# Optimization experiments

Measured on AMD Instinct MI355X. Metric: run time of the kernel, lower is better.

## Reference

```python
import jax, jax.numpy as jnp
import numpy as np

NEG_INF = 1e9  # matches module's -1000000000.0 masking constant


def setup_inputs() -> dict:
    key = jax.random.key(0)
    kq, kv = jax.random.split(key)
    B, T, D = 4, 2048, 1024
    query = jax.random.normal(kq, (B, T, D), dtype=jnp.float32)
    value = jax.random.normal(kv, (B, T, D), dtype=jnp.float32)
    return {"query": query, "value": value}


def reference(query, value):
    # key defaults to value (len(inputs) == 2 path)
    k = value
    # dot-product scores (canonical Keras Attention _calculate_scores)
    scores = jnp.einsum("bqd,bkd->bqk", query, k)  # [B, Tq, Tv]
    Tq, Tv = scores.shape[-2], scores.shape[-1]
    # causal lower-triangular mask over last two dims (row >= col)
    causal_mask = jnp.tril(jnp.ones((Tq, Tv), dtype=bool))  # [Tq, Tv]
    # scores -= 1e9 * (~mask), then softmax (eval mode: no dropout)
    scores = scores - NEG_INF * (~causal_mask).astype(scores.dtype)
    weights = jax.nn.softmax(scores, axis=-1)
    result = jnp.einsum("bqv,bvd->bqd", weights, value)
    return result
```

## Files before the change

### kernel.cpp

```cpp
#include <hip/hip_runtime.h>
#include <hip/hip_fp16.h>

typedef _Float16 half8 __attribute__((ext_vector_type(8)));
typedef float    floatx4 __attribute__((ext_vector_type(4)));
typedef unsigned int uintx4 __attribute__((ext_vector_type(4)));

#define MFMA16(a, b, c) __builtin_amdgcn_mfma_f32_16x16x32_f16((a), (b), (c), 0, 0, 0)

constexpr int T_ = 2048;
constexpr int D_ = 1024;
constexpr int NB = 4;
constexpr int NTILE = 136;
constexpr size_t PT_ELEMS = 16384;

__device__ __forceinline__ half8 cvt8(floatx4 a, floatx4 b) {
  half8 h;
  h[0] = (_Float16)a[0]; h[1] = (_Float16)a[1]; h[2] = (_Float16)a[2]; h[3] = (_Float16)a[3];
  h[4] = (_Float16)b[0]; h[5] = (_Float16)b[1]; h[6] = (_Float16)b[2]; h[7] = (_Float16)b[3];
  return h;
}

__device__ __forceinline__ void gl16(const void* g, void* l) {
  __builtin_amdgcn_global_load_lds(
      (const __attribute__((address_space(1))) void*)g,
      (__attribute__((address_space(3))) void*)l, 16, 0, 0);
}

__global__ __launch_bounds__(256) void cast_h(const float* __restrict__ X,
                                              _Float16* __restrict__ Xh) {
  const size_t i = ((size_t)blockIdx.x * 256 + threadIdx.x) * 8;
  *(half8*)(Xh + i) = cvt8(*(const floatx4*)(X + i), *(const floatx4*)(X + i + 4));
}

__global__ __launch_bounds__(256) void build_vt(const float* __restrict__ V,
                                                _Float16* __restrict__ VhT) {
  __shared__ _Float16 tile[64][65];
  const int bid = blockIdx.x;
  const int b = bid & 3, tt = (bid >> 2) & 31, dd = bid >> 7;
  const float* Vb = V + ((size_t)b * T_ + tt * 64) * D_ + dd * 64;
#pragma unroll
  for (int k = 0; k < 16; ++k) {
    const int e = k * 256 + threadIdx.x, r = e >> 6, c = e & 63;
    tile[r][c] = (_Float16)Vb[(size_t)r * D_ + c];
  }
  __syncthreads();
#pragma unroll
  for (int k = 0; k < 16; ++k) {
    const int e = k * 256 + threadIdx.x, dr = e >> 6, tc = e & 63;
    VhT[((size_t)b * D_ + dd * 64 + dr) * T_ + tt * 64 + tc] = tile[tc][dr];
  }
}

__global__ __launch_bounds__(256, 2) void sgemm(const _Float16* __restrict__ Qh,
                                                const _Float16* __restrict__ Vh,
                                                _Float16* __restrict__ Pt,
                                                float* __restrict__ mg,
                                                float* __restrict__ lg) {
  extern __shared__ __align__(16) char lds[];
  char* As = lds;
  char* Bs = lds + 32768;
  const int tid = threadIdx.x;
  const int w = tid >> 6, l = tid & 63, l15 = l & 15, hi = l >> 4;
  const int wr = (w >> 1) * 64, wc = (w & 1) * 64;

  const int b = (int)(blockIdx.x & 3);
  int rem = (int)(blockIdx.x >> 2), j = 0;
  while (rem >= 16 - j) { rem -= 16 - j; ++j; }
  const int i = j + rem;

  const _Float16* Qb = Qh + ((size_t)(b * T_ + i * 128)) * D_;
  const _Float16* Vb = Vh + ((size_t)(b * T_ + j * 128)) * D_;
  const int srow = w * 32 + (l >> 4);
  char* Adst = As + w * 8192;
  char* Bdst = Bs + w * 8192;

  floatx4 acc[4][4];
#pragma unroll
  for (int mi = 0; mi < 4; ++mi)
#pragma unroll
    for (int ni = 0; ni < 4; ++ni) acc[mi][ni] = (floatx4){0.f, 0.f, 0.f, 0.f};

  for (int s = 0; s < 8; ++s) {
#pragma unroll
    for (int q = 0; q < 8; ++q) {
      const int r0 = srow + q * 4;
      const int sc = ((l & 15) ^ (r0 & 15)) * 8;
      gl16(Qb + (size_t)r0 * D_ + s * 128 + sc, Adst + q * 1024);
      gl16(Vb + (size_t)r0 * D_ + s * 128 + sc, Bdst + q * 1024);
    }
    __syncthreads();
#pragma unroll
    for (int s32 = 0; s32 < 4; ++s32) {
      half8 af[4], bb[4];
#pragma unroll
      for (int mi = 0; mi < 4; ++mi) {
        const int row = wr + mi * 16 + l15;
        af[mi] = *(const half8*)(As + row * 256 + (((s32 * 4 + hi) ^ (row & 15)) << 4));
      }
#pragma unroll
      for (int ni = 0; ni < 4; ++ni) {
        const int row = wc + ni * 16 + l15;
        bb[ni] = *(const half8*)(Bs + row * 256 + (((s32 * 4 + hi) ^ (row & 15)) << 4));
      }
#pragma unroll
      for (int mi = 0; mi < 4; ++mi)
#pragma unroll
        for (int ni = 0; ni < 4; ++ni)
          acc[mi][ni] = MFMA16(af[mi], bb[ni], acc[mi][ni]);
    }
    __syncthreads();
  }

  float* Mex = (float*)Bs;
  float* Lex = (float*)(Bs + 1024);

  if (i == j) {
#pragma unroll
    for (int mi = 0; mi < 4; ++mi)
#pragma unroll
      for (int ni = 0; ni < 4; ++ni) {
        const int col = wc + ni * 16 + l15;
        const int row0 = wr + mi * 16 + 4 * hi;
#pragma unroll
        for (int r = 0; r < 4; ++r)
          if (col > row0 + r) acc[mi][ni][r] = -1e30f;
      }
  }

  floatx4 mrow[4];
#pragma unroll
  for (int mi = 0; mi < 4; ++mi) {
#pragma unroll
    for (int r = 0; r < 4; ++r)
      mrow[mi][r] = fmaxf(fmaxf(acc[mi][0][r], acc[mi][1][r]),
                          fmaxf(acc[mi][2][r], acc[mi][3][r]));
#pragma unroll
    for (int off = 1; off < 16; off <<= 1)
#pragma unroll
      for (int r = 0; r < 4; ++r)
        mrow[mi][r] = fmaxf(mrow[mi][r], __shfl_xor(mrow[mi][r], off));
  }
  if (l15 == 0) {
#pragma unroll
    for (int mi = 0; mi < 4; ++mi)
      *(floatx4*)&Mex[(w & 1) * 128 + wr + mi * 16 + 4 * hi] = mrow[mi];
  }
  __syncthreads();
#pragma unroll
  for (int mi = 0; mi < 4; ++mi) {
    const floatx4 m0 = *(const floatx4*)&Mex[wr + mi * 16 + 4 * hi];
    const floatx4 m1 = *(const floatx4*)&Mex[128 + wr + mi * 16 + 4 * hi];
#pragma unroll
    for (int r = 0; r < 4; ++r) mrow[mi][r] = fmaxf(m0[r], m1[r]);
  }

  floatx4 lsum[4];
#pragma unroll
  for (int mi = 0; mi < 4; ++mi) {
    lsum[mi] = (floatx4){0.f, 0.f, 0.f, 0.f};
    const int row0 = wr + mi * 16 + 4 * hi;
#pragma unroll
    for (int ni = 0; ni < 4; ++ni) {
      const int col = wc + ni * 16 + l15;
#pragma unroll
      for (int r = 0; r < 4; ++r) {
        const float p = __expf(acc[mi][ni][r] - mrow[mi][r]);
        lsum[mi][r] += p;
        *(_Float16*)(As + (row0 + r) * 256 + col * 2) = (_Float16)p;
      }
    }
#pragma unroll
    for (int off = 1; off < 16; off <<= 1)
#pragma unroll
      for (int r = 0; r < 4; ++r) lsum[mi][r] += __shfl_xor(lsum[mi][r], off);
  }
  if (l15 == 0) {
#pragma unroll
    for (int mi = 0; mi < 4; ++mi)
      *(floatx4*)&Lex[(w & 1) * 128 + wr + mi * 16 + 4 * hi] = lsum[mi];
  }
  __syncthreads();

  if (((w & 1) == 0) && l15 == 0) {
    const size_t base = ((size_t)(b * 16 + j)) * 2048 + i * 128;
#pragma unroll
    for (int mi = 0; mi < 4; ++mi) {
      const int r0 = wr + mi * 16 + 4 * hi;
      const floatx4 l0 = *(const floatx4*)&Lex[r0];
      const floatx4 l1 = *(const floatx4*)&Lex[128 + r0];
#pragma unroll
      for (int r = 0; r < 4; ++r) {
        mg[base + r0 + r] = mrow[mi][r];
        lg[base + r0 + r] = l0[r] + l1[r];
      }
    }
  }
  _Float16* Pg = Pt + (size_t)(b * NTILE + ((i * (i + 1)) >> 1) + j) * PT_ELEMS;
  const int drow = tid >> 1, dhalf = tid & 1;
#pragma unroll
  for (int k = 0; k < 8; ++k) {
    const int c = k ^ (tid & 7);
    const uintx4 v = *(const uintx4*)(As + drow * 256 + dhalf * 128 + c * 16);
    *(uintx4*)((char*)Pg + drow * 256 + dhalf * 128 + c * 16) = v;
  }
}

__global__ __launch_bounds__(256) void combine(const float* __restrict__ mg,
                                               const float* __restrict__ lg,
                                               _Float16* __restrict__ ah,
                                               float* __restrict__ linv) {
  const int gid = (int)(blockIdx.x * 256 + threadIdx.x);
  const int b = gid >> 11, row = gid & 2047, i = row >> 7;
  const size_t mb = (size_t)b * 32768 + row;
  float M = -1e30f;
  for (int j = 0; j <= i; ++j) M = fmaxf(M, mg[mb + (size_t)j * 2048]);
  float L = 0.f;
  for (int j = 0; j <= i; ++j) {
    const float a = __expf(mg[mb + (size_t)j * 2048] - M);
    L += a * lg[mb + (size_t)j * 2048];
    ah[((size_t)b * 2048 + row) * 16 + j] = (_Float16)a;
  }
  linv[b * 2048 + row] = 1.0f / L;
}

__global__ __launch_bounds__(256, 2) void pv(const _Float16* __restrict__ Pt,
                                             const _Float16* __restrict__ VhT,
                                             const _Float16* __restrict__ ah,
                                             const float* __restrict__ linv,
                                             float* __restrict__ O) {
  extern __shared__ __align__(16) char lds[];
  char* As = lds;
  char* Bs = lds + 32768;
  const int tid = threadIdx.x;
  const int w = tid >> 6, l = tid & 63, l15 = l & 15, hi = l >> 4;
  const int wr = (w >> 1) * 64, wc = (w & 1) * 64;

  const int b = (int)(blockIdx.x & 3), t = (int)(blockIdx.x >> 2);
  const int r_ = t >> 3;
  const int i = (r_ < 8) ? (15 - r_) : (r_ - 8);
  const int nc = t & 7;
  const int ns = i + 1;

  const _Float16* Pb = Pt + (size_t)(b * NTILE + ((i * (i + 1)) >> 1)) * PT_ELEMS;
  const _Float16* Vt = VhT + ((size_t)(b * D_ + nc * 128)) * T_;
  const int srow = w * 32 + (l >> 4);
  char* Adst = As + w * 8192;
  char* Bdst = Bs + w * 8192;

  floatx4 acc[4][4];
#pragma unroll
  for (int mi = 0; mi < 4; ++mi)
#pragma unroll
    for (int ni = 0; ni < 4; ++ni) acc[mi][ni] = (floatx4){0.f, 0.f, 0.f, 0.f};

  for (int s = 0; s < ns; ++s) {
    _Float16 aw[4];
#pragma unroll
    for (int mi = 0; mi < 4; ++mi)
      aw[mi] = ah[((size_t)(b * 2048 + i * 128 + wr + mi * 16 + l15)) * 16 + s];
#pragma unroll
    for (int q = 0; q < 8; ++q) {
      const int r0 = srow + q * 4;
      const int sc = ((l & 15) ^ (r0 & 15)) * 8;
      gl16(Pb + (size_t)s * PT_ELEMS + (size_t)r0 * 128 + sc, Adst + q * 1024);
      gl16(Vt + (size_t)r0 * T_ + s * 128 + sc, Bdst + q * 1024);
    }
    __syncthreads();
#pragma unroll
    for (int s32 = 0; s32 < 4; ++s32) {
      half8 af[4], bb[4];
#pragma unroll
      for (int mi = 0; mi < 4; ++mi) {
        const int row = wr + mi * 16 + l15;
        af[mi] = *(const half8*)(As + row * 256 + (((s32 * 4 + hi) ^ (row & 15)) << 4));
        af[mi] *= aw[mi];
      }
#pragma unroll
      for (int ni = 0; ni < 4; ++ni) {
        const int row = wc + ni * 16 + l15;
        bb[ni] = *(const half8*)(Bs + row * 256 + (((s32 * 4 + hi) ^ (row & 15)) << 4));
      }
#pragma unroll
      for (int mi = 0; mi < 4; ++mi)
#pragma unroll
        for (int ni = 0; ni < 4; ++ni)
          acc[mi][ni] = MFMA16(af[mi], bb[ni], acc[mi][ni]);
    }
    __syncthreads();
  }

  float* Ob = O + ((size_t)b * T_ + i * 128) * D_ + nc * 128;
#pragma unroll
  for (int mi = 0; mi < 4; ++mi)
#pragma unroll
    for (int r = 0; r < 4; ++r) {
      const int rl = wr + mi * 16 + 4 * hi + r;
      const float iv = linv[b * 2048 + i * 128 + rl];
#pragma unroll
      for (int ni = 0; ni < 4; ++ni)
        Ob[(size_t)rl * D_ + wc + ni * 16 + l15] = acc[mi][ni][r] * iv;
    }
}

__global__ __launch_bounds__(256) void attn_fb(const float* __restrict__ Q,
                                               const float* __restrict__ V,
                                               float* __restrict__ O) {
  __shared__ float sc[2048];
  __shared__ float red[4];
  const int b = (int)(blockIdx.x >> 11), m = (int)(blockIdx.x & 2047);
  const int tid = threadIdx.x;
  const float* Qr = Q + ((size_t)b * T_ + m) * D_;
  for (int kv = tid; kv <= m; kv += 256) {
    const float* Vr = V + ((size_t)b * T_ + kv) * D_;
    float s = 0.f;
    for (int d = 0; d < D_; d += 4) {
      floatx4 q4 = *(const floatx4*)(Qr + d), v4 = *(const floatx4*)(Vr + d);
      s += q4[0] * v4[0] + q4[1] * v4[1] + q4[2] * v4[2] + q4[3] * v4[3];
    }
    sc[kv] = s;
  }
  __syncthreads();
  float mx = -1e30f;
  for (int kv = tid; kv <= m; kv += 256) mx = fmaxf(mx, sc[kv]);
#pragma unroll
  for (int off = 1; off < 64; off <<= 1) mx = fmaxf(mx, __shfl_xor(mx, off));
  if ((tid & 63) == 0) red[tid >> 6] = mx;
  __syncthreads();
  mx = fmaxf(fmaxf(red[0], red[1]), fmaxf(red[2], red[3]));
  __syncthreads();
  float sum = 0.f;
  for (int kv = tid; kv <= m; kv += 256) { float p = __expf(sc[kv] - mx); sc[kv] = p; sum += p; }
#pragma unroll
  for (int off = 1; off < 64; off <<= 1) sum += __shfl_xor(sum, off);
  __syncthreads();
  if ((tid & 63) == 0) red[tid >> 6] = sum;
  __syncthreads();
  const float inv = 1.0f / (red[0] + red[1] + red[2] + red[3]);
  float* Or = O + ((size_t)b * T_ + m) * D_;
  const int d = tid * 4;
  floatx4 o = {0.f, 0.f, 0.f, 0.f};
  for (int kv = 0; kv <= m; ++kv) {
    const float p = sc[kv];
    const floatx4 v4 = *(const floatx4*)(V + ((size_t)b * T_ + kv) * D_ + d);
    o[0] += p * v4[0]; o[1] += p * v4[1]; o[2] += p * v4[2]; o[3] += p * v4[3];
  }
  o[0] *= inv; o[1] *= inv; o[2] *= inv; o[3] *= inv;
  *(floatx4*)(Or + d) = o;
}

extern "C" void kernel_launch(void* const* d_in, const int* in_sizes, int n_in,
                              void* d_out, int out_size, void* d_ws, size_t ws_size,
                              hipStream_t stream) {
  const float* q = (const float*)d_in[0];
  const float* v = (const float*)d_in[1];
  float* out = (float*)d_out;

  const size_t OFF_VH = 16777216;
  const size_t OFF_P  = 33554432;
  const size_t OFF_M  = OFF_P + (size_t)NB * NTILE * PT_ELEMS * 2;
  const size_t OFF_LT = OFF_M + 524288;
  const size_t OFF_AH = OFF_LT + 524288;
  const size_t OFF_LI = OFF_AH + 262144;
  const size_t NEED   = OFF_LI + 32768;

  if (ws_size >= NEED) {
    _Float16* qh = (_Float16*)d_ws;
    _Float16* vh = (_Float16*)((char*)d_ws + OFF_VH);
    _Float16* pt = (_Float16*)((char*)d_ws + OFF_P);
    float* mg = (float*)((char*)d_ws + OFF_M);
    float* lg = (float*)((char*)d_ws + OFF_LT);
    _Float16* ah = (_Float16*)((char*)d_ws + OFF_AH);
    float* li = (float*)((char*)d_ws + OFF_LI);
    hipFuncSetAttribute((const void*)sgemm, hipFuncAttributeMaxDynamicSharedMemorySize, 65536);
    hipFuncSetAttribute((const void*)pv, hipFuncAttributeMaxDynamicSharedMemorySize, 65536);
    cast_h<<<dim3(4096), dim3(256), 0, stream>>>(q, qh);
    cast_h<<<dim3(4096), dim3(256), 0, stream>>>(v, vh);
    sgemm<<<dim3(NB * NTILE), dim3(256), 65536, stream>>>(qh, vh, pt, mg, lg);
    combine<<<dim3(32), dim3(256), 0, stream>>>(mg, lg, ah, li);
    build_vt<<<dim3(2048), dim3(256), 0, stream>>>(v, qh);
    pv<<<dim3(512), dim3(256), 65536, stream>>>(pt, qh, ah, li, out);
  } else {
    attn_fb<<<dim3(NB * T_), dim3(256), 0, stream>>>(q, v, out);
  }
}
```

Before: 118.2 us.

## Shrink PV tiles to 128x64 with smaller k-steps and fuse cast kernels

The two fp16 cast launches are merged into one prep kernel that handles Q and V, with each thread converting 16 elements. The PV kernel moves from 128x128 output tiles with 128-wide k-steps to 128x64 tiles with 64-wide k-steps and static 24KB LDS. That doubles the grid to 1024 blocks, raises the occupancy hint to 4 blocks per SM, and interleaves tile rows to balance causal work. The goal is better occupancy and load balance on the triangular PV work, at the cost of more k-iterations, more barriers and less operand reuse per block.

```diff
diff --git a/kernel.cpp b/kernel.cpp
--- a/kernel.cpp
+++ b/kernel.cpp
@@ -26,10 +26,16 @@
       (__attribute__((address_space(3))) void*)l, 16, 0, 0);
 }
 
-__global__ __launch_bounds__(256) void cast_h(const float* __restrict__ X,
-                                              _Float16* __restrict__ Xh) {
-  const size_t i = ((size_t)blockIdx.x * 256 + threadIdx.x) * 8;
-  *(half8*)(Xh + i) = cvt8(*(const floatx4*)(X + i), *(const floatx4*)(X + i + 4));
+__global__ __launch_bounds__(256) void prep(const float* __restrict__ Q,
+                                            const float* __restrict__ V,
+                                            _Float16* __restrict__ Qh,
+                                            _Float16* __restrict__ Vh) {
+  const int bid = blockIdx.x;
+  const float* src = (bid < 2048) ? Q : V;
+  _Float16* dst = (bid < 2048) ? Qh : Vh;
+  const size_t i = ((size_t)(bid & 2047) * 256 + threadIdx.x) * 16;
+  *(half8*)(dst + i)     = cvt8(*(const floatx4*)(src + i),     *(const floatx4*)(src + i + 4));
+  *(half8*)(dst + i + 8) = cvt8(*(const floatx4*)(src + i + 8), *(const floatx4*)(src + i + 12));
 }
 
 __global__ __launch_bounds__(256) void build_vt(const float* __restrict__ V,
@@ -223,65 +229,69 @@
   linv[b * 2048 + row] = 1.0f / L;
 }
 
-__global__ __launch_bounds__(256, 2) void pv(const _Float16* __restrict__ Pt,
+__global__ __launch_bounds__(256, 4) void pv(const _Float16* __restrict__ Pt,
                                              const _Float16* __restrict__ VhT,
                                              const _Float16* __restrict__ ah,
                                              const float* __restrict__ linv,
                                              float* __restrict__ O) {
-  extern __shared__ __align__(16) char lds[];
-  char* As = lds;
-  char* Bs = lds + 32768;
+  __shared__ __align__(16) char As[16384];
+  __shared__ __align__(16) char Bs[8192];
   const int tid = threadIdx.x;
   const int w = tid >> 6, l = tid & 63, l15 = l & 15, hi = l >> 4;
-  const int wr = (w >> 1) * 64, wc = (w & 1) * 64;
-
-  const int b = (int)(blockIdx.x & 3), t = (int)(blockIdx.x >> 2);
-  const int r_ = t >> 3;
-  const int i = (r_ < 8) ? (15 - r_) : (r_ - 8);
-  const int nc = t & 7;
-  const int ns = i + 1;
-
-  const _Float16* Pb = Pt + (size_t)(b * NTILE + ((i * (i + 1)) >> 1)) * PT_ELEMS;
-  const _Float16* Vt = VhT + ((size_t)(b * D_ + nc * 128)) * T_;
-  const int srow = w * 32 + (l >> 4);
-  char* Adst = As + w * 8192;
-  char* Bdst = Bs + w * 8192;
-
-  floatx4 acc[4][4];
-#pragma unroll
-  for (int mi = 0; mi < 4; ++mi)
+  const int wr = w * 32;
+
+  const int b = (int)(blockIdx.x & 3);
+  const int u = (int)(blockIdx.x >> 2);
+  const int iidx = (u + (u >> 4)) & 15;
+  const int i = (iidx < 8) ? (15 - iidx) : (iidx - 8);
+  const int nc = u >> 4;
+  const int ns = (i + 1) * 2;
+
+  const _Float16* Pp = Pt + (size_t)(b * NTILE + ((i * (i + 1)) >> 1)) * PT_ELEMS;
+  const _Float16* Vt = VhT + ((size_t)(b * D_ + nc * 64)) * T_;
+
+  floatx4 acc[2][4];
+#pragma unroll
+  for (int mi = 0; mi < 2; ++mi)
 #pragma unroll
     for (int ni = 0; ni < 4; ++ni) acc[mi][ni] = (floatx4){0.f, 0.f, 0.f, 0.f};
 
   for (int s = 0; s < ns; ++s) {
-    _Float16 aw[4];
-#pragma unroll
-    for (int mi = 0; mi < 4; ++mi)
-      aw[mi] = ah[((size_t)(b * 2048 + i * 128 + wr + mi * 16 + l15)) * 16 + s];
-#pragma unroll
-    for (int q = 0; q < 8; ++q) {
-      const int r0 = srow + q * 4;
-      const int sc = ((l & 15) ^ (r0 & 15)) * 8;
-      gl16(Pb + (size_t)s * PT_ELEMS + (size_t)r0 * 128 + sc, Adst + q * 1024);
-      gl16(Vt + (size_t)r0 * T_ + s * 128 + sc, Bdst + q * 1024);
+    const int jt = s >> 1, half = s & 1;
+    _Float16 aw[2];
+#pragma unroll
+    for (int mi = 0; mi < 2; ++mi)
+      aw[mi] = ah[((size_t)(b * 2048 + i * 128 + wr + mi * 16 + l15)) * 16 + jt];
+#pragma unroll
+    for (int q = 0; q < 4; ++q) {
+      const int ar = w * 32 + q * 8 + (l >> 3);
+      gl16(Pp + (size_t)jt * PT_ELEMS + (size_t)ar * 128 + half * 64 +
+               ((l & 7) ^ (ar & 7)) * 8,
+           As + w * 4096 + q * 1024);
+    }
+#pragma unroll
+    for (int q = 0; q < 2; ++q) {
+      const int br = w * 16 + q * 8 + (l >> 3);
+      gl16(Vt + (size_t)br * T_ + s * 64 + ((l & 7) ^ (br & 7)) * 8,
+           Bs + w * 2048 + q * 1024);
     }
     __syncthreads();
 #pragma unroll
-    for (int s32 = 0; s32 < 4; ++s32) {
-      half8 af[4], bb[4];
-#pragma unroll
-      for (int mi = 0; mi < 4; ++mi) {
+    for (int s32 = 0; s32 < 2; ++s32) {
+      half8 af[2], bb[4];
+#pragma unroll
+      for (int mi = 0; mi < 2; ++mi) {
         const int row = wr + mi * 16 + l15;
-        af[mi] = *(const half8*)(As + row * 256 + (((s32 * 4 + hi) ^ (row & 15)) << 4));
+        af[mi] = *(const half8*)(As + row * 128 + (((s32 * 4 + hi) ^ (row & 7)) << 4));
         af[mi] *= aw[mi];
       }
 #pragma unroll
       for (int ni = 0; ni < 4; ++ni) {
-        const int row = wc + ni * 16 + l15;
-        bb[ni] = *(const half8*)(Bs + row * 256 + (((s32 * 4 + hi) ^ (row & 15)) << 4));
-      }
-#pragma unroll
-      for (int mi = 0; mi < 4; ++mi)
+        const int row = ni * 16 + l15;
+        bb[ni] = *(const half8*)(Bs + row * 128 + (((s32 * 4 + hi) ^ (row & 7)) << 4));
+      }
+#pragma unroll
+      for (int mi = 0; mi < 2; ++mi)
 #pragma unroll
         for (int ni = 0; ni < 4; ++ni)
           acc[mi][ni] = MFMA16(af[mi], bb[ni], acc[mi][ni]);
@@ -289,16 +299,16 @@
     __syncthreads();
   }
 
-  float* Ob = O + ((size_t)b * T_ + i * 128) * D_ + nc * 128;
-#pragma unroll
-  for (int mi = 0; mi < 4; ++mi)
+  float* Ob = O + ((size_t)b * T_ + i * 128) * D_ + nc * 64;
+#pragma unroll
+  for (int mi = 0; mi < 2; ++mi)
 #pragma unroll
     for (int r = 0; r < 4; ++r) {
       const int rl = wr + mi * 16 + 4 * hi + r;
       const float iv = linv[b * 2048 + i * 128 + rl];
 #pragma unroll
       for (int ni = 0; ni < 4; ++ni)
-        Ob[(size_t)rl * D_ + wc + ni * 16 + l15] = acc[mi][ni][r] * iv;
+        Ob[(size_t)rl * D_ + ni * 16 + l15] = acc[mi][ni][r] * iv;
     }
 }
 
@@ -372,13 +382,11 @@
     _Float16* ah = (_Float16*)((char*)d_ws + OFF_AH);
     float* li = (float*)((char*)d_ws + OFF_LI);
     hipFuncSetAttribute((const void*)sgemm, hipFuncAttributeMaxDynamicSharedMemorySize, 65536);
-    hipFuncSetAttribute((const void*)pv, hipFuncAttributeMaxDynamicSharedMemorySize, 65536);
-    cast_h<<<dim3(4096), dim3(256), 0, stream>>>(q, qh);
-    cast_h<<<dim3(4096), dim3(256), 0, stream>>>(v, vh);
+    prep<<<dim3(4096), dim3(256), 0, stream>>>(q, v, qh, vh);
     sgemm<<<dim3(NB * NTILE), dim3(256), 65536, stream>>>(qh, vh, pt, mg, lg);
     combine<<<dim3(32), dim3(256), 0, stream>>>(mg, lg, ah, li);
     build_vt<<<dim3(2048), dim3(256), 0, stream>>>(v, qh);
-    pv<<<dim3(512), dim3(256), 65536, stream>>>(pt, qh, ah, li, out);
+    pv<<<dim3(1024), dim3(256), 0, stream>>>(pt, qh, ah, li, out);
   } else {
     attn_fb<<<dim3(NB * T_), dim3(256), 0, stream>>>(q, v, out);
   }
```

Result: slower. 120.7 us (+2.1%).

## Fuse Q/V casts into one kernel and halve PV k-step LDS footprint

Applied to the files above, without the earlier changes.

The two fp16 cast launches become one prep kernel in which each thread converts 16 elements. The pv kernel now steps through K in 64-wide chunks instead of 128, so it uses 32 KB of static LDS instead of 64 KB dynamic, and launch bounds allow 3 blocks per CU for more occupancy. The swizzle is adjusted to match 128-byte rows. The trade-off is twice as many loop iterations and barriers per tile, and less data reuse per barrier.

```diff
diff --git a/kernel.cpp b/kernel.cpp
--- a/kernel.cpp
+++ b/kernel.cpp
@@ -26,10 +26,16 @@
       (__attribute__((address_space(3))) void*)l, 16, 0, 0);
 }
 
-__global__ __launch_bounds__(256) void cast_h(const float* __restrict__ X,
-                                              _Float16* __restrict__ Xh) {
-  const size_t i = ((size_t)blockIdx.x * 256 + threadIdx.x) * 8;
-  *(half8*)(Xh + i) = cvt8(*(const floatx4*)(X + i), *(const floatx4*)(X + i + 4));
+__global__ __launch_bounds__(256) void prep(const float* __restrict__ Q,
+                                            const float* __restrict__ V,
+                                            _Float16* __restrict__ Qh,
+                                            _Float16* __restrict__ Vh) {
+  const int bid = blockIdx.x;
+  const float* src = (bid < 2048) ? Q : V;
+  _Float16* dst = (bid < 2048) ? Qh : Vh;
+  const size_t i = ((size_t)(bid & 2047) * 256 + threadIdx.x) * 16;
+  *(half8*)(dst + i)     = cvt8(*(const floatx4*)(src + i),     *(const floatx4*)(src + i + 4));
+  *(half8*)(dst + i + 8) = cvt8(*(const floatx4*)(src + i + 8), *(const floatx4*)(src + i + 12));
 }
 
 __global__ __launch_bounds__(256) void build_vt(const float* __restrict__ V,
@@ -223,29 +229,26 @@
   linv[b * 2048 + row] = 1.0f / L;
 }
 
-__global__ __launch_bounds__(256, 2) void pv(const _Float16* __restrict__ Pt,
+__global__ __launch_bounds__(256, 3) void pv(const _Float16* __restrict__ Pt,
                                              const _Float16* __restrict__ VhT,
                                              const _Float16* __restrict__ ah,
                                              const float* __restrict__ linv,
                                              float* __restrict__ O) {
-  extern __shared__ __align__(16) char lds[];
-  char* As = lds;
-  char* Bs = lds + 32768;
+  __shared__ __align__(16) char As[16384];
+  __shared__ __align__(16) char Bs[16384];
   const int tid = threadIdx.x;
   const int w = tid >> 6, l = tid & 63, l15 = l & 15, hi = l >> 4;
   const int wr = (w >> 1) * 64, wc = (w & 1) * 64;
 
   const int b = (int)(blockIdx.x & 3), t = (int)(blockIdx.x >> 2);
   const int r_ = t >> 3;
-  const int i = (r_ < 8) ? (15 - r_) : (r_ - 8);
+  const int I = (r_ < 8) ? (15 - r_) : (r_ - 8);
   const int nc = t & 7;
-  const int ns = i + 1;
-
-  const _Float16* Pb = Pt + (size_t)(b * NTILE + ((i * (i + 1)) >> 1)) * PT_ELEMS;
+  const int ns = (I + 1) * 2;
+
+  const _Float16* Pp = Pt + (size_t)(b * NTILE + ((I * (I + 1)) >> 1)) * PT_ELEMS;
   const _Float16* Vt = VhT + ((size_t)(b * D_ + nc * 128)) * T_;
-  const int srow = w * 32 + (l >> 4);
-  char* Adst = As + w * 8192;
-  char* Bdst = Bs + w * 8192;
+  const int srow = w * 32 + (l >> 3);
 
   floatx4 acc[4][4];
 #pragma unroll
@@ -254,31 +257,33 @@
     for (int ni = 0; ni < 4; ++ni) acc[mi][ni] = (floatx4){0.f, 0.f, 0.f, 0.f};
 
   for (int s = 0; s < ns; ++s) {
+    const int jt = s >> 1, half = s & 1;
     _Float16 aw[4];
 #pragma unroll
     for (int mi = 0; mi < 4; ++mi)
-      aw[mi] = ah[((size_t)(b * 2048 + i * 128 + wr + mi * 16 + l15)) * 16 + s];
-#pragma unroll
-    for (int q = 0; q < 8; ++q) {
-      const int r0 = srow + q * 4;
-      const int sc = ((l & 15) ^ (r0 & 15)) * 8;
-      gl16(Pb + (size_t)s * PT_ELEMS + (size_t)r0 * 128 + sc, Adst + q * 1024);
-      gl16(Vt + (size_t)r0 * T_ + s * 128 + sc, Bdst + q * 1024);
+      aw[mi] = ah[((size_t)(b * 2048 + I * 128 + wr + mi * 16 + l15)) * 16 + jt];
+#pragma unroll
+    for (int q = 0; q < 4; ++q) {
+      const int ar = srow + q * 8;
+      const int sc = ((l & 7) ^ (ar & 7)) * 8;
+      gl16(Pp + (size_t)jt * PT_ELEMS + (size_t)ar * 128 + half * 64 + sc,
+           As + w * 4096 + q * 1024);
+      gl16(Vt + (size_t)ar * T_ + s * 64 + sc, Bs + w * 4096 + q * 1024);
     }
     __syncthreads();
 #pragma unroll
-    for (int s32 = 0; s32 < 4; ++s32) {
+    for (int s32 = 0; s32 < 2; ++s32) {
       half8 af[4], bb[4];
 #pragma unroll
       for (int mi = 0; mi < 4; ++mi) {
         const int row = wr + mi * 16 + l15;
-        af[mi] = *(const half8*)(As + row * 256 + (((s32 * 4 + hi) ^ (row & 15)) << 4));
+        af[mi] = *(const half8*)(As + row * 128 + (((s32 * 4 + hi) ^ (row & 7)) << 4));
         af[mi] *= aw[mi];
       }
 #pragma unroll
       for (int ni = 0; ni < 4; ++ni) {
         const int row = wc + ni * 16 + l15;
-        bb[ni] = *(const half8*)(Bs + row * 256 + (((s32 * 4 + hi) ^ (row & 15)) << 4));
+        bb[ni] = *(const half8*)(Bs + row * 128 + (((s32 * 4 + hi) ^ (row & 7)) << 4));
       }
 #pragma unroll
       for (int mi = 0; mi < 4; ++mi)
@@ -289,13 +294,13 @@
     __syncthreads();
   }
 
-  float* Ob = O + ((size_t)b * T_ + i * 128) * D_ + nc * 128;
+  float* Ob = O + ((size_t)b * T_ + I * 128) * D_ + nc * 128;
 #pragma unroll
   for (int mi = 0; mi < 4; ++mi)
 #pragma unroll
     for (int r = 0; r < 4; ++r) {
       const int rl = wr + mi * 16 + 4 * hi + r;
-      const float iv = linv[b * 2048 + i * 128 + rl];
+      const float iv = linv[b * 2048 + I * 128 + rl];
 #pragma unroll
       for (int ni = 0; ni < 4; ++ni)
         Ob[(size_t)rl * D_ + wc + ni * 16 + l15] = acc[mi][ni][r] * iv;
@@ -372,13 +377,11 @@
     _Float16* ah = (_Float16*)((char*)d_ws + OFF_AH);
     float* li = (float*)((char*)d_ws + OFF_LI);
     hipFuncSetAttribute((const void*)sgemm, hipFuncAttributeMaxDynamicSharedMemorySize, 65536);
-    hipFuncSetAttribute((const void*)pv, hipFuncAttributeMaxDynamicSharedMemorySize, 65536);
-    cast_h<<<dim3(4096), dim3(256), 0, stream>>>(q, qh);
-    cast_h<<<dim3(4096), dim3(256), 0, stream>>>(v, vh);
+    prep<<<dim3(4096), dim3(256), 0, stream>>>(q, v, qh, vh);
     sgemm<<<dim3(NB * NTILE), dim3(256), 65536, stream>>>(qh, vh, pt, mg, lg);
     combine<<<dim3(32), dim3(256), 0, stream>>>(mg, lg, ah, li);
     build_vt<<<dim3(2048), dim3(256), 0, stream>>>(v, qh);
-    pv<<<dim3(512), dim3(256), 65536, stream>>>(pt, qh, ah, li, out);
+    pv<<<dim3(512), dim3(256), 0, stream>>>(pt, qh, ah, li, out);
   } else {
     attn_fb<<<dim3(NB * T_), dim3(256), 0, stream>>>(q, v, out);
   }
```

After: 127.3 us. 1.08x slower.
